# Performance work log

Measured on AMD Instinct MI355X. Metric: run time of the kernel, lower is better.

Reference implementation:

```python
import jax, jax.numpy as jnp
import numpy as np

B = 8192          # num_envs
OPT = 16          # num options
SHARED = 22       # shared_state_size (hardcoded in module)
UNIQ = 8          # unique_state_size (hardcoded in module)
MIN_DUR, MAX_DUR = 0.1, 0.5  # const.gait_net.valid_swing_duration_range


def _w(k, o, i):
    return jax.random.normal(k, (o, i), jnp.float32) * (1.0 / np.sqrt(i))


def setup_inputs() -> dict:
    key = jax.random.key(0)
    ks = jax.random.split(key, 20)
    obs = jax.random.normal(ks[0], (B, SHARED + OPT * UNIQ), jnp.float32)
    flag = jax.random.uniform(ks[1], (B, OPT)) < 0.25
    u = obs[:, SHARED:].reshape(B, OPT, UNIQ)
    u = u.at[:, :, 0].set(jnp.where(flag, 1.0, u[:, :, 0]))
    obs = jnp.concatenate([obs[:, :SHARED], u.reshape(B, OPT * UNIQ)], axis=1)
    return {
        "obs": obs,
        "sw1": _w(ks[2], 256, 22), "sb1": jnp.zeros((256,), jnp.float32),
        "sw2": _w(ks[3], 256, 256), "sb2": jnp.zeros((256,), jnp.float32),
        "uw1": _w(ks[4], 128, 8), "ub1": jnp.zeros((128,), jnp.float32),
        "uw2": _w(ks[5], 128, 128), "ub2": jnp.zeros((128,), jnp.float32),
        "no_op_embedding": jax.random.normal(ks[6], (128,), jnp.float32),
        "tw1": _w(ks[7], 512, 384), "tb1": jnp.zeros((512,), jnp.float32),
        "tw2": _w(ks[8], 256, 512), "tb2": jnp.zeros((256,), jnp.float32),
        "vw": _w(ks[9], 1, 256), "vb": jnp.zeros((1,), jnp.float32),
        "dw": _w(ks[10], 1, 256), "db": jnp.zeros((1,), jnp.float32),
    }


def reference(obs, sw1, sb1, sw2, sb2, uw1, ub1, uw2, ub2, no_op_embedding,
              tw1, tb1, tw2, tb2, vw, vb, dw, db):
    relu = jax.nn.relu
    shared = obs[:, :SHARED]                               # [B, 22]
    uniq = obs[:, SHARED:].reshape(B, OPT, UNIQ)           # [B, OPT, 8]
    # shared encoder (22 -> 256 -> 256, relu output)
    se = relu(relu(shared @ sw1.T + sb1) @ sw2.T + sb2)    # [B, 256]
    # unique encoder applied to all options at once (8 -> 128 -> 128)
    ue = relu(relu(uniq @ uw1.T + ub1) @ uw2.T + ub2)      # [B, OPT, 128]
    no_op = uniq[:, :, 0] == 1.0                           # [B, OPT]
    ue = jnp.where(no_op[..., None], no_op_embedding, ue)
    trunk_in = jnp.concatenate(
        [jnp.broadcast_to(se[:, None, :], (B, OPT, se.shape[-1])), ue], axis=-1)
    t = relu(relu(trunk_in @ tw1.T + tb1) @ tw2.T + tb2)   # [B, OPT, 256]
    logits = (t @ vw.T + vb).squeeze(-1)                   # [B, OPT]
    duration = jax.nn.sigmoid((t @ dw.T + db).squeeze(-1)) * (MAX_DUR - MIN_DUR) + MIN_DUR
    return logits, duration
```

## Files before the change

### kernel.cpp

```cpp
#include <hip/hip_runtime.h>
#include <stdint.h>


static constexpr int B_ = 8192;

typedef __attribute__((ext_vector_type(8))) short bf16x8;
typedef __attribute__((ext_vector_type(4))) float f32x4;

__device__ __forceinline__ float u2f(uint16_t u) {
    union { uint32_t i; float f; } c; c.i = (uint32_t)u << 16; return c.f;
}
__device__ __forceinline__ uint16_t f2u(float f) {
    union { float f; uint32_t i; } c; c.f = f;
    uint32_t x = c.i;
    return (uint16_t)((x + 0x7FFFu + ((x >> 16) & 1u)) >> 16);
}

static constexpr size_t WCSE   = 0;
static constexpr size_t WTW1SE = 4194304;
static constexpr size_t WTW1UE = WTW1SE + 131072;
static constexpr size_t WTW2   = WTW1UE + 65536;
static constexpr size_t WUW2   = WTW2 + 131072;
static constexpr size_t WSW2   = WUW2 + 16384;

__global__ __launch_bounds__(256) void k_conv(
    const float* __restrict__ tw1, const float* __restrict__ tw2,
    const float* __restrict__ uw2, const float* __restrict__ sw2,
    uint16_t* __restrict__ ws)
{
    int i4 = blockIdx.x * 256 + threadIdx.x;
    const float* src; size_t dst;
    if (i4 < 32768) {
        int g = i4 * 4, n = g >> 8, k = g & 255;
        src = tw1 + (size_t)n * 384 + k;
        dst = WTW1SE + (size_t)g;
    } else if (i4 < 49152) {
        int q = i4 - 32768, n = q >> 5, w = q & 31;
        src = tw1 + (size_t)n * 384 + 256 + w * 4;
        dst = WTW1UE + (size_t)n * 128 + w * 4;
    } else if (i4 < 81920) {
        int q = (i4 - 49152) * 4;
        src = tw2 + q; dst = WTW2 + q;
    } else if (i4 < 86016) {
        int q = (i4 - 81920) * 4;
        src = uw2 + q; dst = WUW2 + q;
    } else {
        int q = (i4 - 86016) * 4;
        src = sw2 + q; dst = WSW2 + q;
    }
    float4 v = *reinterpret_cast<const float4*>(src);
    ushort4 o;
    o.x = f2u(v.x); o.y = f2u(v.y); o.z = f2u(v.z); o.w = f2u(v.w);
    *reinterpret_cast<ushort4*>(ws + dst) = o;
}

__global__ __launch_bounds__(256) void k_cse(
    const float* __restrict__ obs,
    const float* __restrict__ sw1, const float* __restrict__ sb1,
    const float* __restrict__ sb2, const float* __restrict__ tb1,
    uint16_t* __restrict__ ws)
{
    __shared__ float xs[16][24];
    __shared__ uint16_t h1s[16 * 264];
    __shared__ uint16_t seL[16 * 264];
    const int t = threadIdx.x;
    const int b0 = blockIdx.x * 16;
    const uint16_t* sw2b   = ws + WSW2;
    const uint16_t* tw1seb = ws + WTW1SE;

    for (int i = t; i < 352; i += 256) {
        int e = i / 22, c = i - e * 22;
        xs[e][c] = obs[(size_t)(b0 + e) * 150 + c];
    }
    __syncthreads();
    {
        float w[22];
        #pragma unroll
        for (int k = 0; k < 22; ++k) w[k] = sw1[t * 22 + k];
        const float bias = sb1[t];
        #pragma unroll
        for (int e = 0; e < 16; ++e) {
            float a = bias;
            #pragma unroll
            for (int k = 0; k < 22; ++k) a += w[k] * xs[e][k];
            h1s[e * 264 + t] = f2u(fmaxf(a, 0.f));
        }
    }
    __syncthreads();
    const int wv = t >> 6, lane = t & 63, quad = lane >> 4, l16 = lane & 15;
    {
        f32x4 acc[4];
        #pragma unroll
        for (int nt = 0; nt < 4; ++nt) {
            float bv = sb2[wv * 64 + nt * 16 + l16];
            acc[nt] = {bv, bv, bv, bv};
        }
        const uint16_t* bb = sw2b + (size_t)(wv * 64 + l16) * 256 + quad * 8;
        bf16x8 bc[4], bn[4];
        #pragma unroll
        for (int nt = 0; nt < 4; ++nt)
            bc[nt] = *reinterpret_cast<const bf16x8*>(bb + nt * 4096);
        #pragma unroll
        for (int kk = 0; kk < 8; ++kk) {
            if (kk < 7) {
                #pragma unroll
                for (int nt = 0; nt < 4; ++nt)
                    bn[nt] = *reinterpret_cast<const bf16x8*>(
                        bb + nt * 4096 + (kk + 1) * 32);
            }
            bf16x8 af = *reinterpret_cast<const bf16x8*>(
                &h1s[l16 * 264 + kk * 32 + quad * 8]);
            #pragma unroll
            for (int nt = 0; nt < 4; ++nt)
                acc[nt] = __builtin_amdgcn_mfma_f32_16x16x32_bf16(
                    af, bc[nt], acc[nt], 0, 0, 0);
            #pragma unroll
            for (int nt = 0; nt < 4; ++nt) bc[nt] = bn[nt];
        }
        #pragma unroll
        for (int nt = 0; nt < 4; ++nt)
            #pragma unroll
            for (int r = 0; r < 4; ++r)
                seL[(quad * 4 + r) * 264 + wv * 64 + nt * 16 + l16] =
                    f2u(fmaxf(acc[nt][r], 0.f));
    }
    __syncthreads();
    {
        f32x4 acc[8];
        #pragma unroll
        for (int nt = 0; nt < 8; ++nt) {
            float bv = tb1[wv * 128 + nt * 16 + l16];
            acc[nt] = {bv, bv, bv, bv};
        }
        const uint16_t* bb = tw1seb + (size_t)(wv * 128 + l16) * 256 + quad * 8;
        bf16x8 bc[8], bn[8];
        #pragma unroll
        for (int nt = 0; nt < 8; ++nt)
            bc[nt] = *reinterpret_cast<const bf16x8*>(bb + nt * 4096);
        #pragma unroll
        for (int kk = 0; kk < 8; ++kk) {
            if (kk < 7) {
                #pragma unroll
                for (int nt = 0; nt < 8; ++nt)
                    bn[nt] = *reinterpret_cast<const bf16x8*>(
                        bb + nt * 4096 + (kk + 1) * 32);
            }
            bf16x8 af = *reinterpret_cast<const bf16x8*>(
                &seL[l16 * 264 + kk * 32 + quad * 8]);
            #pragma unroll
            for (int nt = 0; nt < 8; ++nt)
                acc[nt] = __builtin_amdgcn_mfma_f32_16x16x32_bf16(
                    af, bc[nt], acc[nt], 0, 0, 0);
            #pragma unroll
            for (int nt = 0; nt < 8; ++nt) bc[nt] = bn[nt];
        }
        #pragma unroll
        for (int nt = 0; nt < 8; ++nt)
            #pragma unroll
            for (int r = 0; r < 4; ++r)
                ws[WCSE + (size_t)(b0 + quad * 4 + r) * 512 +
                   wv * 128 + nt * 16 + l16] = f2u(acc[nt][r]);
    }
}

static constexpr int UQ_OFF   = 0;
static constexpr int NOOP_OFF = 2112;
static constexpr int CSE_OFF  = 2368;
static constexpr int H1U_OFF  = 6464;
static constexpr int UET_OFF  = 23872;
static constexpr int H1T_OFF  = 41280;
static constexpr int SMEM_SZ  = 75072;

__global__ __launch_bounds__(512, 4) void k_main(
    const float* __restrict__ obs,
    const float* __restrict__ uw1, const float* __restrict__ ub1,
    const float* __restrict__ ub2, const float* __restrict__ emb,
    const float* __restrict__ tb2,
    const float* __restrict__ vw,  const float* __restrict__ vb,
    const float* __restrict__ dw,  const float* __restrict__ db,
    const uint16_t* __restrict__ wsb,
    float* __restrict__ out)
{
    __shared__ __align__(16) char smem[SMEM_SZ];
    float*    uq    = (float*)(smem + UQ_OFF);
    float*    noopf = (float*)(smem + NOOP_OFF);
    uint16_t* cseL  = (uint16_t*)(smem + CSE_OFF);
    uint16_t* h1u   = (uint16_t*)(smem + H1U_OFF);
    uint16_t* uet   = (uint16_t*)(smem + UET_OFF);
    uint16_t* h1t   = (uint16_t*)(smem + H1T_OFF);
    uint16_t* t2    = h1t;

    const int t    = threadIdx.x;
    const int wv   = t >> 6;
    const int lane = t & 63;
    const int quad = lane >> 4;
    const int l16  = lane & 15;
    const int b0   = blockIdx.x * 4;

    const uint16_t* csep  = wsb + WCSE;
    const uint16_t* tw1ue = wsb + WTW1UE;
    const uint16_t* tw2b  = wsb + WTW2;
    const uint16_t* uw2b  = wsb + WUW2;

    {
        int e = t >> 7, c = t & 127;
        uq[e * 132 + c] = obs[(size_t)(b0 + e) * 150 + 22 + c];
        #pragma unroll
        for (int ii = 0; ii < 2; ++ii) {
            int i = t + ii * 512;
            int ee = i >> 8, cc = i & 255;
            ((uint32_t*)cseL)[ee * 256 + cc] =
                ((const uint32_t*)(csep + (size_t)(b0 + ee) * 512))[cc];
        }
        if (t < 64) {
            int ee = t >> 4, o = t & 15;
            noopf[t] = (obs[(size_t)(b0 + ee) * 150 + 22 + o * 8] == 1.0f) ? 1.0f : 0.0f;
        }
    }
    __syncthreads();

    {
        const int n = t & 127, h = t >> 7;
        float w[8];
        #pragma unroll
        for (int k = 0; k < 8; ++k) w[k] = uw1[n * 8 + k];
        const float bias = ub1[n];
        #pragma unroll
        for (int ii = 0; ii < 16; ++ii) {
            int row = h * 16 + ii;
            const float4* xp = (const float4*)&uq[h * 132 + ii * 8];
            float4 xa = xp[0], xb = xp[1];
            float a = bias + w[0] * xa.x + w[1] * xa.y + w[2] * xa.z + w[3] * xa.w
                           + w[4] * xb.x + w[5] * xb.y + w[6] * xb.z + w[7] * xb.w;
            h1u[row * 136 + n] = f2u(fmaxf(a, 0.f));
        }
    }
    __syncthreads();

    {
        const int n = wv * 16 + l16;
        const float bv = ub2[n];
        const float ev = emb[n];
        f32x4 acc[4];
        #pragma unroll
        for (int mt = 0; mt < 4; ++mt) acc[mt] = {bv, bv, bv, bv};
        #pragma unroll
        for (int kk = 0; kk < 4; ++kk) {
            bf16x8 bf = *reinterpret_cast<const bf16x8*>(
                &uw2b[(size_t)n * 128 + kk * 32 + quad * 8]);
            #pragma unroll
            for (int mt = 0; mt < 4; ++mt) {
                bf16x8 af = *reinterpret_cast<const bf16x8*>(
                    &h1u[(mt * 16 + l16) * 136 + kk * 32 + quad * 8]);
                acc[mt] = __builtin_amdgcn_mfma_f32_16x16x32_bf16(af, bf, acc[mt], 0, 0, 0);
            }
        }
        #pragma unroll
        for (int mt = 0; mt < 4; ++mt)
            #pragma unroll
            for (int r = 0; r < 4; ++r) {
                int row = mt * 16 + quad * 4 + r;
                float v = (noopf[row] != 0.0f) ? ev : fmaxf(acc[mt][r], 0.f);
                uet[row * 136 + n] = f2u(v);
            }
    }
    __syncthreads();

    f32x4 acc2[4][2];
    #pragma unroll
    for (int nt = 0; nt < 2; ++nt) {
        float bv = tb2[wv * 32 + nt * 16 + l16];
        #pragma unroll
        for (int mt = 0; mt < 4; ++mt) acc2[mt][nt] = {bv, bv, bv, bv};
    }

    #pragma unroll
    for (int nc = 0; nc < 2; ++nc) {
        {
            f32x4 acc1[4][2];
            #pragma unroll
            for (int nt = 0; nt < 2; ++nt) {
                int n = nc * 256 + wv * 32 + nt * 16 + l16;
                #pragma unroll
                for (int mt = 0; mt < 4; ++mt) {
                    float v = u2f(cseL[mt * 512 + n]);
                    acc1[mt][nt] = {v, v, v, v};
                }
            }
            const uint16_t* bb = tw1ue + (size_t)(nc * 256 + wv * 32 + l16) * 128
                                 + quad * 8;
            bf16x8 bc[2], bn[2];
            bc[0] = *reinterpret_cast<const bf16x8*>(bb);
            bc[1] = *reinterpret_cast<const bf16x8*>(bb + 2048);
            #pragma unroll
            for (int kk = 0; kk < 4; ++kk) {
                if (kk < 3) {
                    bn[0] = *reinterpret_cast<const bf16x8*>(bb + (kk + 1) * 32);
                    bn[1] = *reinterpret_cast<const bf16x8*>(bb + 2048 + (kk + 1) * 32);
                }
                bf16x8 af[4];
                #pragma unroll
                for (int mt = 0; mt < 4; ++mt)
                    af[mt] = *reinterpret_cast<const bf16x8*>(
                        &uet[(mt * 16 + l16) * 136 + kk * 32 + quad * 8]);
                #pragma unroll
                for (int mt = 0; mt < 4; ++mt)
                    #pragma unroll
                    for (int nt = 0; nt < 2; ++nt)
                        acc1[mt][nt] = __builtin_amdgcn_mfma_f32_16x16x32_bf16(
                            af[mt], bc[nt], acc1[mt][nt], 0, 0, 0);
                bc[0] = bn[0]; bc[1] = bn[1];
            }
            #pragma unroll
            for (int mt = 0; mt < 4; ++mt)
                #pragma unroll
                for (int nt = 0; nt < 2; ++nt)
                    #pragma unroll
                    for (int r = 0; r < 4; ++r) {
                        int row = mt * 16 + quad * 4 + r;
                        h1t[row * 264 + wv * 32 + nt * 16 + l16] =
                            f2u(fmaxf(acc1[mt][nt][r], 0.f));
                    }
        }
        __syncthreads();
        {
            const uint16_t* cb = tw2b + (size_t)(wv * 32 + l16) * 512 + nc * 256
                                 + quad * 8;
            bf16x8 cc[2], cn[2];
            cc[0] = *reinterpret_cast<const bf16x8*>(cb);
            cc[1] = *reinterpret_cast<const bf16x8*>(cb + 8192);
            #pragma unroll
            for (int k2 = 0; k2 < 8; ++k2) {
                if (k2 < 7) {
                    cn[0] = *reinterpret_cast<const bf16x8*>(cb + (k2 + 1) * 32);
                    cn[1] = *reinterpret_cast<const bf16x8*>(cb + 8192 + (k2 + 1) * 32);
                }
                bf16x8 af[4];
                #pragma unroll
                for (int mt = 0; mt < 4; ++mt)
                    af[mt] = *reinterpret_cast<const bf16x8*>(
                        &h1t[(mt * 16 + l16) * 264 + k2 * 32 + quad * 8]);
                #pragma unroll
                for (int mt = 0; mt < 4; ++mt)
                    #pragma unroll
                    for (int nt = 0; nt < 2; ++nt)
                        acc2[mt][nt] = __builtin_amdgcn_mfma_f32_16x16x32_bf16(
                            af[mt], cc[nt], acc2[mt][nt], 0, 0, 0);
                cc[0] = cn[0]; cc[1] = cn[1];
            }
        }
        if (nc == 0) __syncthreads();
    }
    __syncthreads();
    #pragma unroll
    for (int mt = 0; mt < 4; ++mt)
        #pragma unroll
        for (int nt = 0; nt < 2; ++nt)
            #pragma unroll
            for (int r = 0; r < 4; ++r) {
                int row = mt * 16 + quad * 4 + r;
                t2[row * 264 + wv * 32 + nt * 16 + l16] =
                    f2u(fmaxf(acc2[mt][nt][r], 0.f));
            }
    __syncthreads();

    {
        float vwf[4], dwf[4];
        #pragma unroll
        for (int j = 0; j < 4; ++j) {
            vwf[j] = vw[lane + 64 * j];
            dwf[j] = dw[lane + 64 * j];
        }
        const float vbf = vb[0], dbf = db[0];
        #pragma unroll
        for (int rr = 0; rr < 8; ++rr) {
            int row = wv * 8 + rr;
            float sv = 0.f, sd = 0.f;
            #pragma unroll
            for (int j = 0; j < 4; ++j) {
                float tv = u2f(t2[row * 264 + lane + 64 * j]);
                sv += tv * vwf[j];
                sd += tv * dwf[j];
            }
            #pragma unroll
            for (int off = 32; off > 0; off >>= 1) {
                sv += __shfl_down(sv, off);
                sd += __shfl_down(sd, off);
            }
            if (lane == 0) {
                int g = blockIdx.x * 64 + row;
                out[g] = sv + vbf;
                float z = sd + dbf;
                float sig = 1.f / (1.f + __expf(-z));
                out[B_ * 16 + g] = sig * 0.4f + 0.1f;
            }
        }
    }
}

extern "C" void kernel_launch(void* const* d_in, const int* in_sizes, int n_in,
                              void* d_out, int out_size, void* d_ws, size_t ws_size,
                              hipStream_t stream) {
    const float* obs = (const float*)d_in[0];
    const float* sw1 = (const float*)d_in[1];
    const float* sb1 = (const float*)d_in[2];
    const float* sw2 = (const float*)d_in[3];
    const float* sb2 = (const float*)d_in[4];
    const float* uw1 = (const float*)d_in[5];
    const float* ub1 = (const float*)d_in[6];
    const float* uw2 = (const float*)d_in[7];
    const float* ub2 = (const float*)d_in[8];
    const float* emb = (const float*)d_in[9];
    const float* tw1 = (const float*)d_in[10];
    const float* tb1 = (const float*)d_in[11];
    const float* tw2 = (const float*)d_in[12];
    const float* tb2 = (const float*)d_in[13];
    const float* vw  = (const float*)d_in[14];
    const float* vb  = (const float*)d_in[15];
    const float* dw  = (const float*)d_in[16];
    const float* db  = (const float*)d_in[17];

    uint16_t* wsb = (uint16_t*)d_ws;

    k_conv<<<400, 256, 0, stream>>>(tw1, tw2, uw2, sw2, wsb);
    k_cse<<<512, 256, 0, stream>>>(obs, sw1, sb1, sb2, tb1, wsb);
    k_main<<<B_ / 4, 512, 0, stream>>>(obs, uw1, ub1, ub2, emb, tb2,
                                       vw, vb, dw, db, wsb, (float*)d_out);
}
```

Before: 241.9 us.

## Use MFMA for unique-encoder first layer and widen shared-encoder blocks

The unique encoder's first layer (8->128) moves from scalar FMAs to bf16 MFMA. Its input is converted to bf16 with K zero-padded to 32, and uw1 is pre-converted and padded in the conversion kernel. Separately, the shared-encoder kernel goes from 256 to 512 threads so each wave computes a narrower slice of output columns, which adds parallelism per block. The cost is some wasted MFMA work on the zero padding and bf16 rounding of raw observations in the first layer.

```diff
diff --git a/kernel.cpp b/kernel.cpp
--- a/kernel.cpp
+++ b/kernel.cpp
@@ -22,13 +22,25 @@
 static constexpr size_t WTW2   = WTW1UE + 65536;
 static constexpr size_t WUW2   = WTW2 + 131072;
 static constexpr size_t WSW2   = WUW2 + 16384;
+static constexpr size_t WUW1B  = WSW2 + 65536;
 
 __global__ __launch_bounds__(256) void k_conv(
     const float* __restrict__ tw1, const float* __restrict__ tw2,
     const float* __restrict__ uw2, const float* __restrict__ sw2,
-    uint16_t* __restrict__ ws)
+    const float* __restrict__ uw1, uint16_t* __restrict__ ws)
 {
     int i4 = blockIdx.x * 256 + threadIdx.x;
+    if (i4 >= 102400) {
+        int q = i4 - 102400;
+        int n = q >> 3, k0 = (q & 7) * 4;
+        ushort4 o = {0, 0, 0, 0};
+        if (k0 < 8) {
+            float4 v = *reinterpret_cast<const float4*>(uw1 + n * 8 + k0);
+            o.x = f2u(v.x); o.y = f2u(v.y); o.z = f2u(v.z); o.w = f2u(v.w);
+        }
+        *reinterpret_cast<ushort4*>(ws + WUW1B + n * 32 + k0) = o;
+        return;
+    }
     const float* src; size_t dst;
     if (i4 < 32768) {
         int g = i4 * 4, n = g >> 8, k = g & 255;
@@ -54,7 +66,7 @@
     *reinterpret_cast<ushort4*>(ws + dst) = o;
 }
 
-__global__ __launch_bounds__(256) void k_cse(
+__global__ __launch_bounds__(512) void k_cse(
     const float* __restrict__ obs,
     const float* __restrict__ sw1, const float* __restrict__ sb1,
     const float* __restrict__ sb2, const float* __restrict__ tb1,
@@ -68,34 +80,69 @@
     const uint16_t* sw2b   = ws + WSW2;
     const uint16_t* tw1seb = ws + WTW1SE;
 
-    for (int i = t; i < 352; i += 256) {
-        int e = i / 22, c = i - e * 22;
+    if (t < 352) {
+        int e = t / 22, c = t - e * 22;
         xs[e][c] = obs[(size_t)(b0 + e) * 150 + c];
     }
     __syncthreads();
     {
+        const int n = t & 255;
         float w[22];
         #pragma unroll
-        for (int k = 0; k < 22; ++k) w[k] = sw1[t * 22 + k];
-        const float bias = sb1[t];
-        #pragma unroll
-        for (int e = 0; e < 16; ++e) {
+        for (int k = 0; k < 22; ++k) w[k] = sw1[n * 22 + k];
+        const float bias = sb1[n];
+        #pragma unroll
+        for (int ii = 0; ii < 8; ++ii) {
+            int e = (t >> 8) * 8 + ii;
             float a = bias;
             #pragma unroll
             for (int k = 0; k < 22; ++k) a += w[k] * xs[e][k];
-            h1s[e * 264 + t] = f2u(fmaxf(a, 0.f));
+            h1s[e * 264 + n] = f2u(fmaxf(a, 0.f));
         }
     }
     __syncthreads();
     const int wv = t >> 6, lane = t & 63, quad = lane >> 4, l16 = lane & 15;
     {
+        f32x4 acc[2];
+        #pragma unroll
+        for (int nt = 0; nt < 2; ++nt) {
+            float bv = sb2[wv * 32 + nt * 16 + l16];
+            acc[nt] = {bv, bv, bv, bv};
+        }
+        const uint16_t* bb = sw2b + (size_t)(wv * 32 + l16) * 256 + quad * 8;
+        bf16x8 bc[2], bn[2];
+        bc[0] = *reinterpret_cast<const bf16x8*>(bb);
+        bc[1] = *reinterpret_cast<const bf16x8*>(bb + 4096);
+        #pragma unroll
+        for (int kk = 0; kk < 8; ++kk) {
+            if (kk < 7) {
+                bn[0] = *reinterpret_cast<const bf16x8*>(bb + (kk + 1) * 32);
+                bn[1] = *reinterpret_cast<const bf16x8*>(bb + 4096 + (kk + 1) * 32);
+            }
+            bf16x8 af = *reinterpret_cast<const bf16x8*>(
+                &h1s[l16 * 264 + kk * 32 + quad * 8]);
+            #pragma unroll
+            for (int nt = 0; nt < 2; ++nt)
+                acc[nt] = __builtin_amdgcn_mfma_f32_16x16x32_bf16(
+                    af, bc[nt], acc[nt], 0, 0, 0);
+            bc[0] = bn[0]; bc[1] = bn[1];
+        }
+        #pragma unroll
+        for (int nt = 0; nt < 2; ++nt)
+            #pragma unroll
+            for (int r = 0; r < 4; ++r)
+                seL[(quad * 4 + r) * 264 + wv * 32 + nt * 16 + l16] =
+                    f2u(fmaxf(acc[nt][r], 0.f));
+    }
+    __syncthreads();
+    {
         f32x4 acc[4];
         #pragma unroll
         for (int nt = 0; nt < 4; ++nt) {
-            float bv = sb2[wv * 64 + nt * 16 + l16];
+            float bv = tb1[wv * 64 + nt * 16 + l16];
             acc[nt] = {bv, bv, bv, bv};
         }
-        const uint16_t* bb = sw2b + (size_t)(wv * 64 + l16) * 256 + quad * 8;
+        const uint16_t* bb = tw1seb + (size_t)(wv * 64 + l16) * 256 + quad * 8;
         bf16x8 bc[4], bn[4];
         #pragma unroll
         for (int nt = 0; nt < 4; ++nt)
@@ -109,7 +156,7 @@
                         bb + nt * 4096 + (kk + 1) * 32);
             }
             bf16x8 af = *reinterpret_cast<const bf16x8*>(
-                &h1s[l16 * 264 + kk * 32 + quad * 8]);
+                &seL[l16 * 264 + kk * 32 + quad * 8]);
             #pragma unroll
             for (int nt = 0; nt < 4; ++nt)
                 acc[nt] = __builtin_amdgcn_mfma_f32_16x16x32_bf16(
@@ -121,59 +168,22 @@
         for (int nt = 0; nt < 4; ++nt)
             #pragma unroll
             for (int r = 0; r < 4; ++r)
-                seL[(quad * 4 + r) * 264 + wv * 64 + nt * 16 + l16] =
-                    f2u(fmaxf(acc[nt][r], 0.f));
-    }
-    __syncthreads();
-    {
-        f32x4 acc[8];
-        #pragma unroll
-        for (int nt = 0; nt < 8; ++nt) {
-            float bv = tb1[wv * 128 + nt * 16 + l16];
-            acc[nt] = {bv, bv, bv, bv};
-        }
-        const uint16_t* bb = tw1seb + (size_t)(wv * 128 + l16) * 256 + quad * 8;
-        bf16x8 bc[8], bn[8];
-        #pragma unroll
-        for (int nt = 0; nt < 8; ++nt)
-            bc[nt] = *reinterpret_cast<const bf16x8*>(bb + nt * 4096);
-        #pragma unroll
-        for (int kk = 0; kk < 8; ++kk) {
-            if (kk < 7) {
-                #pragma unroll
-                for (int nt = 0; nt < 8; ++nt)
-                    bn[nt] = *reinterpret_cast<const bf16x8*>(
-                        bb + nt * 4096 + (kk + 1) * 32);
-            }
-            bf16x8 af = *reinterpret_cast<const bf16x8*>(
-                &seL[l16 * 264 + kk * 32 + quad * 8]);
-            #pragma unroll
-            for (int nt = 0; nt < 8; ++nt)
-                acc[nt] = __builtin_amdgcn_mfma_f32_16x16x32_bf16(
-                    af, bc[nt], acc[nt], 0, 0, 0);
-            #pragma unroll
-            for (int nt = 0; nt < 8; ++nt) bc[nt] = bn[nt];
-        }
-        #pragma unroll
-        for (int nt = 0; nt < 8; ++nt)
-            #pragma unroll
-            for (int r = 0; r < 4; ++r)
                 ws[WCSE + (size_t)(b0 + quad * 4 + r) * 512 +
-                   wv * 128 + nt * 16 + l16] = f2u(acc[nt][r]);
-    }
-}
-
-static constexpr int UQ_OFF   = 0;
-static constexpr int NOOP_OFF = 2112;
-static constexpr int CSE_OFF  = 2368;
-static constexpr int H1U_OFF  = 6464;
-static constexpr int UET_OFF  = 23872;
-static constexpr int H1T_OFF  = 41280;
-static constexpr int SMEM_SZ  = 75072;
+                   wv * 64 + nt * 16 + l16] = f2u(acc[nt][r]);
+    }
+}
+
+static constexpr int UQB_OFF  = 0;
+static constexpr int NOOP_OFF = 5120;
+static constexpr int CSE_OFF  = 5376;
+static constexpr int H1U_OFF  = 9472;
+static constexpr int UET_OFF  = 26880;
+static constexpr int H1T_OFF  = 44288;
+static constexpr int SMEM_SZ  = 78080;
 
 __global__ __launch_bounds__(512, 4) void k_main(
     const float* __restrict__ obs,
-    const float* __restrict__ uw1, const float* __restrict__ ub1,
+    const float* __restrict__ ub1,
     const float* __restrict__ ub2, const float* __restrict__ emb,
     const float* __restrict__ tb2,
     const float* __restrict__ vw,  const float* __restrict__ vb,
@@ -182,7 +192,7 @@
     float* __restrict__ out)
 {
     __shared__ __align__(16) char smem[SMEM_SZ];
-    float*    uq    = (float*)(smem + UQ_OFF);
+    uint16_t* uqb   = (uint16_t*)(smem + UQB_OFF);
     float*    noopf = (float*)(smem + NOOP_OFF);
     uint16_t* cseL  = (uint16_t*)(smem + CSE_OFF);
     uint16_t* h1u   = (uint16_t*)(smem + H1U_OFF);
@@ -201,10 +211,19 @@
     const uint16_t* tw1ue = wsb + WTW1UE;
     const uint16_t* tw2b  = wsb + WTW2;
     const uint16_t* uw2b  = wsb + WUW2;
-
-    {
-        int e = t >> 7, c = t & 127;
-        uq[e * 132 + c] = obs[(size_t)(b0 + e) * 150 + 22 + c];
+    const uint16_t* uw1b  = wsb + WUW1B;
+
+    {
+        int r = t >> 3, q = t & 7;
+        int e = r >> 4, o = r & 15;
+        ushort4 ov = {0, 0, 0, 0};
+        if (q < 2) {
+            const float2* sp = reinterpret_cast<const float2*>(
+                &obs[(size_t)(b0 + e) * 150 + 22 + o * 8 + q * 4]);
+            float2 a = sp[0], b = sp[1];
+            ov.x = f2u(a.x); ov.y = f2u(a.y); ov.z = f2u(b.x); ov.w = f2u(b.y);
+        }
+        *reinterpret_cast<ushort4*>(&uqb[r * 40 + q * 4]) = ov;
         #pragma unroll
         for (int ii = 0; ii < 2; ++ii) {
             int i = t + ii * 512;
@@ -213,27 +232,32 @@
                 ((const uint32_t*)(csep + (size_t)(b0 + ee) * 512))[cc];
         }
         if (t < 64) {
-            int ee = t >> 4, o = t & 15;
-            noopf[t] = (obs[(size_t)(b0 + ee) * 150 + 22 + o * 8] == 1.0f) ? 1.0f : 0.0f;
-        }
-    }
-    __syncthreads();
-
-    {
-        const int n = t & 127, h = t >> 7;
-        float w[8];
-        #pragma unroll
-        for (int k = 0; k < 8; ++k) w[k] = uw1[n * 8 + k];
-        const float bias = ub1[n];
-        #pragma unroll
-        for (int ii = 0; ii < 16; ++ii) {
-            int row = h * 16 + ii;
-            const float4* xp = (const float4*)&uq[h * 132 + ii * 8];
-            float4 xa = xp[0], xb = xp[1];
-            float a = bias + w[0] * xa.x + w[1] * xa.y + w[2] * xa.z + w[3] * xa.w
-                           + w[4] * xb.x + w[5] * xb.y + w[6] * xb.z + w[7] * xb.w;
-            h1u[row * 136 + n] = f2u(fmaxf(a, 0.f));
-        }
+            int ee = t >> 4, oo = t & 15;
+            noopf[t] = (obs[(size_t)(b0 + ee) * 150 + 22 + oo * 8] == 1.0f) ? 1.0f : 0.0f;
+        }
+    }
+    __syncthreads();
+
+    {
+        const int n = wv * 16 + l16;
+        const float bv = ub1[n];
+        f32x4 acc[4];
+        #pragma unroll
+        for (int mt = 0; mt < 4; ++mt) acc[mt] = {bv, bv, bv, bv};
+        bf16x8 bf = *reinterpret_cast<const bf16x8*>(&uw1b[n * 32 + quad * 8]);
+        #pragma unroll
+        for (int mt = 0; mt < 4; ++mt) {
+            bf16x8 af = *reinterpret_cast<const bf16x8*>(
+                &uqb[(mt * 16 + l16) * 40 + quad * 8]);
+            acc[mt] = __builtin_amdgcn_mfma_f32_16x16x32_bf16(af, bf, acc[mt], 0, 0, 0);
+        }
+        #pragma unroll
+        for (int mt = 0; mt < 4; ++mt)
+            #pragma unroll
+            for (int r = 0; r < 4; ++r) {
+                int row = mt * 16 + quad * 4 + r;
+                h1u[row * 136 + n] = f2u(fmaxf(acc[mt][r], 0.f));
+            }
     }
     __syncthreads();
 
@@ -422,8 +446,8 @@
 
     uint16_t* wsb = (uint16_t*)d_ws;
 
-    k_conv<<<400, 256, 0, stream>>>(tw1, tw2, uw2, sw2, wsb);
-    k_cse<<<512, 256, 0, stream>>>(obs, sw1, sb1, sb2, tb1, wsb);
-    k_main<<<B_ / 4, 512, 0, stream>>>(obs, uw1, ub1, ub2, emb, tb2,
+    k_conv<<<404, 256, 0, stream>>>(tw1, tw2, uw2, sw2, uw1, wsb);
+    k_cse<<<512, 512, 0, stream>>>(obs, sw1, sb1, sb2, tb1, wsb);
+    k_main<<<B_ / 4, 512, 0, stream>>>(obs, ub1, ub2, emb, tb2,
                                        vw, vb, dw, db, wsb, (float*)d_out);
 }
```

New measurement: 238.5 us (median of 2 runs). No clear change (-1.4%).
